# Kernel tuning notes

Measured on AMD Instinct MI355X. Metric: run time of the kernel, lower is better.

The kernel has to match this reference:

```python
import jax, jax.numpy as jnp
import numpy as np

VOCAB = 32000
B, S = 1, 2048
D = 1024          # emb_dim == qkv_dim
H = 16            # num_heads
HD = D // H       # head_dim = 64
M = 4096          # mlp_dim
L = 4             # num_layers
WIN = 512         # sliding_window_size
HALF = WIN // 2   # attend to |i-j| <= HALF
N_GLOBAL = 64
EPS = 1e-6


def sinusoidal_pos_emb(max_len, d, max_scale=10000.0):
    pos = np.arange(max_len)[:, None].astype(np.float32)
    div = np.exp(np.arange(0, d, 2).astype(np.float32) * (-np.log(max_scale) / d))
    pe = np.zeros((max_len, d), dtype=np.float32)
    pe[:, 0::2] = np.sin(pos * div)
    pe[:, 1::2] = np.cos(pos * div)
    return jnp.asarray(pe)


def layer_norm(x, scale, bias):
    mu = jnp.mean(x, axis=-1, keepdims=True)
    var = jnp.mean(jnp.square(x - mu), axis=-1, keepdims=True)
    return (x - mu) * jax.lax.rsqrt(var + EPS) * scale + bias


def setup_inputs() -> dict:
    key = jax.random.key(0)
    ks = jax.random.split(key, 16)
    inputs = jax.random.randint(ks[0], (B, S), 0, VOCAB, dtype=jnp.int32)
    gm = jnp.zeros((B, S), dtype=bool).at[:, :N_GLOBAL].set(True)
    std = 0.02
    return {
        'inputs': inputs,
        'global_mask': gm,
        'embed': jax.random.normal(ks[1], (VOCAB, D), jnp.float32),
        'wq': jax.random.normal(ks[2], (L, D, H, HD), jnp.float32) * std,
        'wk': jax.random.normal(ks[3], (L, D, H, HD), jnp.float32) * std,
        'wv': jax.random.normal(ks[4], (L, D, H, HD), jnp.float32) * std,
        'wo': jax.random.normal(ks[5], (L, H, HD, D), jnp.float32) * std,
        'ln1_s': jnp.ones((L, D), jnp.float32),
        'ln1_b': jnp.zeros((L, D), jnp.float32),
        'ln2_s': jnp.ones((L, D), jnp.float32),
        'ln2_b': jnp.zeros((L, D), jnp.float32),
        'w1': jax.random.normal(ks[6], (L, D, M), jnp.float32) * std,
        'b1': jnp.zeros((L, M), jnp.float32),
        'w2': jax.random.normal(ks[7], (L, M, D), jnp.float32) * std,
        'b2': jnp.zeros((L, D), jnp.float32),
        'lnf_s': jnp.ones((D,), jnp.float32),
        'lnf_b': jnp.zeros((D,), jnp.float32),
    }


def _attention_mask(global_mask):
    idx = jnp.arange(S)
    band = jnp.abs(idx[:, None] - idx[None, :]) <= HALF           # [S, S]
    allowed = band[None, :, :] | global_mask[:, :, None] | global_mask[:, None, :]
    return allowed[:, None, :, :]                                  # [B, 1, S, S]


def forward(inputs, global_mask, embed, wq, wk, wv, wo, ln1_s, ln1_b,
            ln2_s, ln2_b, w1, b1, w2, b2, lnf_s, lnf_b):
    x = embed[inputs]                                # [B, S, D]
    x = x + sinusoidal_pos_emb(S, D)[None]
    mask = _attention_mask(global_mask)              # [B, 1, S, S]
    neg = jnp.asarray(-1e9, x.dtype)
    scale = 1.0 / jnp.sqrt(jnp.asarray(HD, x.dtype))
    for l in range(L):
        h = layer_norm(x, ln1_s[l], ln1_b[l])
        q = jnp.einsum('bsd,dhk->bshk', h, wq[l]) * scale
        k = jnp.einsum('bsd,dhk->bshk', h, wk[l])
        v = jnp.einsum('bsd,dhk->bshk', h, wv[l])
        scores = jnp.einsum('bqhk,bshk->bhqs', q, k)         # [B, H, S, S]
        scores = jnp.where(mask, scores, neg)
        probs = jax.nn.softmax(scores, axis=-1)
        ctx = jnp.einsum('bhqs,bshk->bqhk', probs, v)
        attn_out = jnp.einsum('bqhk,hkd->bqd', ctx, wo[l])
        x = x + attn_out
        y = layer_norm(x, ln2_s[l], ln2_b[l])
        y = jax.nn.relu(jnp.einsum('bsd,dm->bsm', y, w1[l]) + b1[l])
        y = jnp.einsum('bsm,md->bsd', y, w2[l]) + b2[l]
        x = x + y
    return layer_norm(x, lnf_s, lnf_b)


def reference(inputs, global_mask, embed, wq, wk, wv, wo, ln1_s, ln1_b,
              ln2_s, ln2_b, w1, b1, w2, b2, lnf_s, lnf_b):
    return forward(inputs, global_mask, embed, wq, wk, wv, wo, ln1_s, ln1_b,
                   ln2_s, ln2_b, w1, b1, w2, b2, lnf_s, lnf_b)
```

## Files before the change

kernel.cpp:

```cpp
#include <hip/hip_runtime.h>
#include <hip/hip_bf16.h>

typedef __attribute__((ext_vector_type(8))) short bf16x8;
typedef __attribute__((ext_vector_type(4))) float f32x4;

__device__ __forceinline__ ushort f2bf(float f) {
    union { float f; uint u; } v; v.f = f;
    uint r = v.u + 0x7FFF + ((v.u >> 16) & 1);
    return (ushort)(r >> 16);
}

__device__ __forceinline__ void ld16(const void* g, void* l) {
    __builtin_amdgcn_global_load_lds(
        (const __attribute__((address_space(1))) void*)g,
        (__attribute__((address_space(3))) void*)l, 16, 0, 0);
}

__global__ __launch_bounds__(256) void conv_w_kernel(
    const float* __restrict__ src, ushort* __restrict__ dst,
    int K, int N, float scale)
{
    __shared__ ushort Ts[64][65];
    const int tid = threadIdx.x;
    const int n0 = blockIdx.x * 64;
    const int k0 = blockIdx.y * 64;
    const int c4 = tid & 15;
    const int r0 = tid >> 4;
    #pragma unroll
    for (int it = 0; it < 4; it++) {
        int r = r0 + it * 16;
        float4 v = *(const float4*)(src + (size_t)(k0 + r) * N + n0 + c4 * 4);
        Ts[c4 * 4 + 0][r] = f2bf(v.x * scale);
        Ts[c4 * 4 + 1][r] = f2bf(v.y * scale);
        Ts[c4 * 4 + 2][r] = f2bf(v.z * scale);
        Ts[c4 * 4 + 3][r] = f2bf(v.w * scale);
    }
    __syncthreads();
    #pragma unroll
    for (int it = 0; it < 4; it++) {
        int nr = r0 + it * 16;
        uint lo = (uint)Ts[nr][c4 * 4 + 0] | ((uint)Ts[nr][c4 * 4 + 1] << 16);
        uint hi = (uint)Ts[nr][c4 * 4 + 2] | ((uint)Ts[nr][c4 * 4 + 3] << 16);
        uint2 w = make_uint2(lo, hi);
        *(uint2*)(dst + (size_t)(n0 + nr) * K + k0 + c4 * 4) = w;
    }
}

template<int TN>
__global__ __launch_bounds__(256) void gemm_t(
    const ushort* __restrict__ A, const ushort* __restrict__ Bt,
    const float* __restrict__ bias, const float* resid,
    float* outF, ushort* outB, int M, int N, int K, int relu)
{
    __shared__ ushort As[4][128 * 32];
    __shared__ ushort Bs[4][TN * 32];
    const int tid  = threadIdx.x;
    const int lane = tid & 63;
    const int wave = tid >> 6;
    const int quad = lane >> 4;
    const int lr   = lane & 15;
    const int wm   = wave >> 1;
    const int wn   = wave & 1;
    constexpr int NT = (TN == 128) ? 4 : 2;
    const int bm0 = blockIdx.x * 128;
    const int bn0 = blockIdx.y * TN;

    f32x4 acc[4][NT];
    #pragma unroll
    for (int i = 0; i < 4; i++)
        #pragma unroll
        for (int j = 0; j < NT; j++)
            acc[i][j] = (f32x4){0.f, 0.f, 0.f, 0.f};

    const ushort* gA = A  + (size_t)(bm0 + (tid >> 2)) * K + (tid & 3) * 8;
    const ushort* gB = Bt + (size_t)(bn0 + (tid >> 2)) * K + (tid & 3) * 8;

    auto stage = [&](int b, int k) {
        ushort* la = &As[b][wave * 512];
        ushort* lb = &Bs[b][wave * 512];
        ld16(gA + k, la);
        ld16(gA + k + (size_t)64 * K, la + 2048);
        ld16(gB + k, lb);
        if constexpr (TN == 128) ld16(gB + k + (size_t)64 * K, lb + 2048);
    };
    auto step = [&](int b, int t3) {
        bf16x8 aF[4], bF[NT];
        const ushort* as = As[b];
        const ushort* bs = Bs[b];
        #pragma unroll
        for (int mt = 0; mt < 4; mt++)
            aF[mt] = *(const bf16x8*)&as[(wm * 64 + mt * 16 + lr) * 32 + quad * 8];
        #pragma unroll
        for (int nt = 0; nt < NT; nt++)
            bF[nt] = *(const bf16x8*)&bs[(wn * (TN / 2) + nt * 16 + lr) * 32 + quad * 8];
        if (t3 >= 0) stage(t3 & 3, t3 * 32);
        #pragma unroll
        for (int mt = 0; mt < 4; mt++)
            #pragma unroll
            for (int nt = 0; nt < NT; nt++)
                acc[mt][nt] = __builtin_amdgcn_mfma_f32_16x16x32_bf16(
                    aF[mt], bF[nt], acc[mt][nt], 0, 0, 0);
    };

    const int ntk = K >> 5;
    stage(0, 0); stage(1, 32); stage(2, 64);
    for (int t = 0; t < ntk - 2; ++t) {
        if constexpr (TN == 128) asm volatile("s_waitcnt vmcnt(8)" ::: "memory");
        else                     asm volatile("s_waitcnt vmcnt(6)" ::: "memory");
        __builtin_amdgcn_s_barrier();
        step(t & 3, (t + 3 < ntk) ? (t + 3) : -1);
    }
    if constexpr (TN == 128) asm volatile("s_waitcnt vmcnt(4)" ::: "memory");
    else                     asm volatile("s_waitcnt vmcnt(3)" ::: "memory");
    __builtin_amdgcn_s_barrier();
    step((ntk - 2) & 3, -1);
    asm volatile("s_waitcnt vmcnt(0)" ::: "memory");
    __builtin_amdgcn_s_barrier();
    step((ntk - 1) & 3, -1);

    #pragma unroll
    for (int mt = 0; mt < 4; mt++) {
        #pragma unroll
        for (int nt = 0; nt < NT; nt++) {
            int col  = bn0 + wn * (TN / 2) + nt * 16 + lr;
            int rowb = bm0 + wm * 64 + mt * 16 + quad * 4;
            #pragma unroll
            for (int r = 0; r < 4; r++) {
                int row = rowb + r;
                float v = acc[mt][nt][r];
                if (bias)  v += bias[col];
                if (resid) v += resid[(size_t)row * N + col];
                if (relu)  v = fmaxf(v, 0.f);
                if (outF)  outF[(size_t)row * N + col] = v;
                else       outB[(size_t)row * N + col] = f2bf(v);
            }
        }
    }
}

#define LDA 72

__global__ __launch_bounds__(256) void attn_mfma_kernel(
    const ushort* __restrict__ qkv, ushort* __restrict__ Cm,
    float* __restrict__ po, float* __restrict__ pm, float* __restrict__ pl)
{
    const int bx   = blockIdx.x;
    const int h    = blockIdx.y;
    const int sp   = (bx >= 31);
    const int qt   = sp ? 0 : bx + 1;
    const int s    = sp ? bx - 31 : 0;
    const int tid  = threadIdx.x;
    const int lane = tid & 63;
    const int wave = tid >> 6;
    const int quad = lane >> 4;
    const int lr   = lane & 15;
    const int q0   = qt * 64;

    __shared__ ushort Qs[64 * LDA];
    __shared__ ushort Ks[64 * LDA];
    __shared__ ushort Vt[64 * LDA];
    __shared__ ushort Ps[64 * LDA];

    {
        int ql = tid >> 2, d0 = (tid & 3) * 16;
        const ushort* qp = qkv + (size_t)(q0 + ql) * 3072 + h * 64 + d0;
        *(uint4*)&Qs[ql * LDA + d0]     = *(const uint4*)qp;
        *(uint4*)&Qs[ql * LDA + d0 + 8] = *(const uint4*)(qp + 8);
    }
    __syncthreads();

    bf16x8 aQ[2];
    #pragma unroll
    for (int kc = 0; kc < 2; kc++)
        aQ[kc] = *(const bf16x8*)&Qs[(wave * 16 + lr) * LDA + kc * 32 + quad * 8];

    f32x4 o[4];
    #pragma unroll
    for (int nt = 0; nt < 4; nt++) o[nt] = (f32x4){0.f, 0.f, 0.f, 0.f};
    float m_[4], l_[4];
    #pragma unroll
    for (int r = 0; r < 4; r++) { m_[r] = -1e30f; l_[r] = 0.f; }

    int kt0 = 0, kt1 = 0, ntiles;
    if (sp) {
        ntiles = 8;
    } else {
        kt0 = qt - 4; if (kt0 < 1)  kt0 = 1;
        kt1 = qt + 4; if (kt1 > 31) kt1 = 31;
        ntiles = 1 + (kt1 - kt0 + 1);
    }

    for (int idx = 0; idx < ntiles; idx++) {
        int kt, maskF;
        if (sp) { kt = s * 8 + idx; maskF = 0; }
        else if (idx == 0) { kt = 0; maskF = 0; }
        else { kt = kt0 + idx - 1; maskF = (kt == qt - 4) || (kt == qt + 4); }

        __syncthreads();

        {
            int kl = tid >> 2, d0 = (tid & 3) * 16;
            const ushort* kp = qkv + (size_t)(kt * 64 + kl) * 3072 + 1024 + h * 64 + d0;
            *(uint4*)&Ks[kl * LDA + d0]     = *(const uint4*)kp;
            *(uint4*)&Ks[kl * LDA + d0 + 8] = *(const uint4*)(kp + 8);
        }
        {
            int kp2 = tid & 31, dc = tid >> 5, d0v = dc * 8;
            const ushort* vp = qkv + (size_t)(kt * 64 + 2 * kp2) * 3072 + 2048 + h * 64 + d0v;
            ushort va[8], vb[8];
            *(uint4*)va = *(const uint4*)vp;
            *(uint4*)vb = *(const uint4*)(vp + 3072);
            #pragma unroll
            for (int i = 0; i < 8; i++) {
                uint w = (uint)va[i] | ((uint)vb[i] << 16);
                *(uint*)&Vt[(d0v + i) * LDA + 2 * kp2] = w;
            }
        }
        __syncthreads();

        f32x4 sAcc[4];
        #pragma unroll
        for (int nt = 0; nt < 4; nt++) sAcc[nt] = (f32x4){0.f, 0.f, 0.f, 0.f};
        #pragma unroll
        for (int kc = 0; kc < 2; kc++) {
            #pragma unroll
            for (int nt = 0; nt < 4; nt++) {
                bf16x8 bK = *(const bf16x8*)&Ks[(nt * 16 + lr) * LDA + kc * 32 + quad * 8];
                sAcc[nt] = __builtin_amdgcn_mfma_f32_16x16x32_bf16(aQ[kc], bK, sAcc[nt], 0, 0, 0);
            }
        }

        if (maskF) {
            #pragma unroll
            for (int nt = 0; nt < 4; nt++) {
                int j = kt * 64 + lr + nt * 16;
                #pragma unroll
                for (int r = 0; r < 4; r++) {
                    int q = q0 + wave * 16 + quad * 4 + r;
                    int d = q - j; if (d < 0) d = -d;
                    if (d > 256) sAcc[nt][r] = -1e30f;
                }
            }
        }

        float rmax[4];
        #pragma unroll
        for (int r = 0; r < 4; r++) {
            float v = fmaxf(fmaxf(sAcc[0][r], sAcc[1][r]), fmaxf(sAcc[2][r], sAcc[3][r]));
            v = fmaxf(v, __shfl_xor(v, 1));
            v = fmaxf(v, __shfl_xor(v, 2));
            v = fmaxf(v, __shfl_xor(v, 4));
            v = fmaxf(v, __shfl_xor(v, 8));
            rmax[r] = v;
        }
        float alpha[4];
        #pragma unroll
        for (int r = 0; r < 4; r++) {
            float mn = fmaxf(m_[r], rmax[r]);
            alpha[r] = __expf(m_[r] - mn);
            m_[r] = mn;
        }
        float psum[4] = {0.f, 0.f, 0.f, 0.f};
        #pragma unroll
        for (int nt = 0; nt < 4; nt++)
            #pragma unroll
            for (int r = 0; r < 4; r++) {
                float p = __expf(sAcc[nt][r] - m_[r]);
                sAcc[nt][r] = p;
                psum[r] += p;
            }
        #pragma unroll
        for (int r = 0; r < 4; r++) {
            float v = psum[r];
            v += __shfl_xor(v, 1);
            v += __shfl_xor(v, 2);
            v += __shfl_xor(v, 4);
            v += __shfl_xor(v, 8);
            l_[r] = l_[r] * alpha[r] + v;
        }
        #pragma unroll
        for (int nt = 0; nt < 4; nt++)
            #pragma unroll
            for (int r = 0; r < 4; r++)
                o[nt][r] *= alpha[r];

        #pragma unroll
        for (int nt = 0; nt < 4; nt++)
            #pragma unroll
            for (int r = 0; r < 4; r++)
                Ps[(wave * 16 + quad * 4 + r) * LDA + lr + nt * 16] = f2bf(sAcc[nt][r]);
        __syncthreads();

        #pragma unroll
        for (int kc = 0; kc < 2; kc++) {
            bf16x8 aP = *(const bf16x8*)&Ps[(wave * 16 + lr) * LDA + kc * 32 + quad * 8];
            #pragma unroll
            for (int nt = 0; nt < 4; nt++) {
                bf16x8 bV = *(const bf16x8*)&Vt[(nt * 16 + lr) * LDA + kc * 32 + quad * 8];
                o[nt] = __builtin_amdgcn_mfma_f32_16x16x32_bf16(aP, bV, o[nt], 0, 0, 0);
            }
        }
    }

    if (!sp) {
        #pragma unroll
        for (int nt = 0; nt < 4; nt++) {
            int dim = lr + nt * 16;
            #pragma unroll
            for (int r = 0; r < 4; r++) {
                int row = q0 + wave * 16 + quad * 4 + r;
                Cm[(size_t)row * 1024 + h * 64 + dim] = f2bf(o[nt][r] / l_[r]);
            }
        }
    } else {
        const int base = (h * 4 + s) * 64;
        #pragma unroll
        for (int nt = 0; nt < 4; nt++) {
            int dim = lr + nt * 16;
            #pragma unroll
            for (int r = 0; r < 4; r++) {
                int row = wave * 16 + quad * 4 + r;
                po[(size_t)(base + row) * 64 + dim] = o[nt][r];
            }
        }
        if (lr == 0) {
            #pragma unroll
            for (int r = 0; r < 4; r++) {
                int row = wave * 16 + quad * 4 + r;
                pm[base + row] = m_[r];
                pl[base + row] = l_[r];
            }
        }
    }
}

__global__ __launch_bounds__(256) void attn_combine_kernel(
    const float* __restrict__ po, const float* __restrict__ pm,
    const float* __restrict__ pl, ushort* __restrict__ Cm)
{
    const int h   = blockIdx.x;
    const int tid = threadIdx.x;
    const int row = tid >> 2;
    const int d0  = (tid & 3) * 16;
    float m[4], l[4];
    #pragma unroll
    for (int s = 0; s < 4; s++) {
        m[s] = pm[(h * 4 + s) * 64 + row];
        l[s] = pl[(h * 4 + s) * 64 + row];
    }
    float M = fmaxf(fmaxf(m[0], m[1]), fmaxf(m[2], m[3]));
    float w[4], L = 0.f;
    #pragma unroll
    for (int s = 0; s < 4; s++) { w[s] = __expf(m[s] - M); L += l[s] * w[s]; }
    float inv = 1.0f / L;
    #pragma unroll
    for (int dd = 0; dd < 16; dd += 4) {
        float a0 = 0.f, a1 = 0.f, a2 = 0.f, a3 = 0.f;
        #pragma unroll
        for (int s = 0; s < 4; s++) {
            float4 v = *(const float4*)&po[(size_t)((h * 4 + s) * 64 + row) * 64 + d0 + dd];
            a0 += v.x * w[s]; a1 += v.y * w[s]; a2 += v.z * w[s]; a3 += v.w * w[s];
        }
        ushort* out = &Cm[(size_t)row * 1024 + h * 64 + d0 + dd];
        out[0] = f2bf(a0 * inv); out[1] = f2bf(a1 * inv);
        out[2] = f2bf(a2 * inv); out[3] = f2bf(a3 * inv);
    }
}

__global__ __launch_bounds__(256) void ln_kernel(
    const float* __restrict__ X, const float* __restrict__ gs,
    const float* __restrict__ gb, ushort* outB, float* outF)
{
    const int row = blockIdx.x;
    const int tid = threadIdx.x;
    const int lane = tid & 63;
    const int wave = tid >> 6;
    __shared__ float red[8];

    const float* x = X + (size_t)row * 1024;
    float4 v = *(const float4*)(x + tid * 4);
    float s1 = v.x + v.y + v.z + v.w;
    float s2 = v.x * v.x + v.y * v.y + v.z * v.z + v.w * v.w;
    #pragma unroll
    for (int off = 32; off > 0; off >>= 1) {
        s1 += __shfl_down(s1, off);
        s2 += __shfl_down(s2, off);
    }
    if (lane == 0) { red[wave] = s1; red[4 + wave] = s2; }
    __syncthreads();
    float S1 = red[0] + red[1] + red[2] + red[3];
    float S2 = red[4] + red[5] + red[6] + red[7];
    float mu  = S1 * (1.0f / 1024.0f);
    float var = S2 * (1.0f / 1024.0f) - mu * mu;
    float inv = rsqrtf(var + 1e-6f);
    const float* vp = (const float*)&v;
    #pragma unroll
    for (int i = 0; i < 4; i++) {
        int d = tid * 4 + i;
        float val = (vp[i] - mu) * inv * gs[d] + gb[d];
        if (outF) outF[(size_t)row * 1024 + d] = val;
        else      outB[(size_t)row * 1024 + d] = f2bf(val);
    }
}

__global__ __launch_bounds__(256) void embed_kernel(
    const int* __restrict__ ids, const float* __restrict__ emb,
    float* __restrict__ x)
{
    const int row = blockIdx.x;
    const int tid = threadIdx.x;
    const int id  = ids[row];
    const float c = 0.0089944731f;
    #pragma unroll
    for (int i = 0; i < 4; i++) {
        int d  = tid * 4 + i;
        int de = d & ~1;
        float dv  = __expf(-c * (float)de);
        float ang = (float)row * dv;
        float pe  = (d & 1) ? cosf(ang) : sinf(ang);
        x[(size_t)row * 1024 + d] = emb[(size_t)id * 1024 + d] + pe;
    }
}

extern "C" void kernel_launch(void* const* d_in, const int* in_sizes, int n_in,
                              void* d_out, int out_size, void* d_ws, size_t ws_size,
                              hipStream_t stream)
{
    const int*   ids   = (const int*)d_in[0];
    const float* embed = (const float*)d_in[2];
    const float* wq    = (const float*)d_in[3];
    const float* wk    = (const float*)d_in[4];
    const float* wv    = (const float*)d_in[5];
    const float* wo    = (const float*)d_in[6];
    const float* ln1s  = (const float*)d_in[7];
    const float* ln1b  = (const float*)d_in[8];
    const float* ln2s  = (const float*)d_in[9];
    const float* ln2b  = (const float*)d_in[10];
    const float* w1    = (const float*)d_in[11];
    const float* b1    = (const float*)d_in[12];
    const float* w2    = (const float*)d_in[13];
    const float* b2    = (const float*)d_in[14];
    const float* lnfs  = (const float*)d_in[15];
    const float* lnfb  = (const float*)d_in[16];

    char* ws = (char*)d_ws;
    float*  x   = (float*)ws;
    ushort* h   = (ushort*)(ws + (size_t)(8  << 20));
    ushort* qkv = (ushort*)(ws + (size_t)(12 << 20));
    ushort* ctx = (ushort*)(ws + (size_t)(24 << 20));
    ushort* wb  = (ushort*)(ws + (size_t)(28 << 20));
    float*  po  = (float*)(ws + (size_t)(8  << 20));
    float*  pm  = (float*)(ws + (size_t)(9  << 20));
    float*  pl  = (float*)(ws + (size_t)(9  << 20) + (1 << 16));
    ushort* y1  = qkv;

    const dim3 blk(256);

    embed_kernel<<<2048, blk, 0, stream>>>(ids, embed, x);

    for (int l = 0; l < 4; l++) {
        const float* wq_l = wq + (size_t)l * 1024 * 1024;
        const float* wk_l = wk + (size_t)l * 1024 * 1024;
        const float* wv_l = wv + (size_t)l * 1024 * 1024;
        const float* wo_l = wo + (size_t)l * 1024 * 1024;
        const float* w1_l = w1 + (size_t)l * 1024 * 4096;
        const float* w2_l = w2 + (size_t)l * 4096 * 1024;

        ln_kernel<<<2048, blk, 0, stream>>>(x, ln1s + l * 1024, ln1b + l * 1024, h, nullptr);

        conv_w_kernel<<<dim3(16, 16), blk, 0, stream>>>(wq_l, wb,                1024, 1024, 0.125f);
        conv_w_kernel<<<dim3(16, 16), blk, 0, stream>>>(wk_l, wb + 1024 * 1024,  1024, 1024, 1.0f);
        conv_w_kernel<<<dim3(16, 16), blk, 0, stream>>>(wv_l, wb + 2048 * 1024,  1024, 1024, 1.0f);
        gemm_t<128><<<dim3(16, 24), blk, 0, stream>>>(h, wb, nullptr, nullptr,
                                                      nullptr, qkv, 2048, 3072, 1024, 0);

        attn_mfma_kernel<<<dim3(35, 16), blk, 0, stream>>>(qkv, ctx, po, pm, pl);
        attn_combine_kernel<<<dim3(16), blk, 0, stream>>>(po, pm, pl, ctx);

        conv_w_kernel<<<dim3(16, 16), blk, 0, stream>>>(wo_l, wb, 1024, 1024, 1.0f);
        gemm_t<64><<<dim3(16, 16), blk, 0, stream>>>(ctx, wb, nullptr, x,
                                                     x, nullptr, 2048, 1024, 1024, 0);

        ln_kernel<<<2048, blk, 0, stream>>>(x, ln2s + l * 1024, ln2b + l * 1024, h, nullptr);

        conv_w_kernel<<<dim3(64, 16), blk, 0, stream>>>(w1_l, wb, 1024, 4096, 1.0f);
        gemm_t<128><<<dim3(16, 32), blk, 0, stream>>>(h, wb, b1 + (size_t)l * 4096, nullptr,
                                                      nullptr, y1, 2048, 4096, 1024, 1);

        conv_w_kernel<<<dim3(16, 64), blk, 0, stream>>>(w2_l, wb, 4096, 1024, 1.0f);
        gemm_t<64><<<dim3(16, 16), blk, 0, stream>>>(y1, wb, b2 + (size_t)l * 1024, x,
                                                     x, nullptr, 2048, 1024, 4096, 0);
    }

    ln_kernel<<<2048, blk, 0, stream>>>(x, lnfs, lnfb, nullptr, (float*)d_out);
}
```

Before: 1.151 ms.

## Split-K the output-projection and MLP-down GEMMs with a separate reduction kernel

The N=1024 GEMMs (attention output projection and second MLP matmul) launched only 256 blocks. They now split K across blockIdx.z (2 and 4 ways) and write fp32 partials to a workspace buffer. A new reduction kernel sums the partials and adds bias and the residual. This raises block count to fill more CUs, at the cost of extra partial-sum traffic and one more launch per GEMM.

```diff
diff --git a/kernel.cpp b/kernel.cpp
--- a/kernel.cpp
+++ b/kernel.cpp
@@ -50,7 +50,8 @@
 __global__ __launch_bounds__(256) void gemm_t(
     const ushort* __restrict__ A, const ushort* __restrict__ Bt,
     const float* __restrict__ bias, const float* resid,
-    float* outF, ushort* outB, int M, int N, int K, int relu)
+    float* outF, ushort* outB, int M, int N, int K, int ldk, int relu,
+    float* __restrict__ outP)
 {
     __shared__ ushort As[4][128 * 32];
     __shared__ ushort Bs[4][TN * 32];
@@ -64,6 +65,7 @@
     constexpr int NT = (TN == 128) ? 4 : 2;
     const int bm0 = blockIdx.x * 128;
     const int bn0 = blockIdx.y * TN;
+    const int kz  = blockIdx.z * K;
 
     f32x4 acc[4][NT];
     #pragma unroll
@@ -72,16 +74,16 @@
         for (int j = 0; j < NT; j++)
             acc[i][j] = (f32x4){0.f, 0.f, 0.f, 0.f};
 
-    const ushort* gA = A  + (size_t)(bm0 + (tid >> 2)) * K + (tid & 3) * 8;
-    const ushort* gB = Bt + (size_t)(bn0 + (tid >> 2)) * K + (tid & 3) * 8;
+    const ushort* gA = A  + (size_t)(bm0 + (tid >> 2)) * ldk + kz + (tid & 3) * 8;
+    const ushort* gB = Bt + (size_t)(bn0 + (tid >> 2)) * ldk + kz + (tid & 3) * 8;
 
     auto stage = [&](int b, int k) {
         ushort* la = &As[b][wave * 512];
         ushort* lb = &Bs[b][wave * 512];
         ld16(gA + k, la);
-        ld16(gA + k + (size_t)64 * K, la + 2048);
+        ld16(gA + k + (size_t)64 * ldk, la + 2048);
         ld16(gB + k, lb);
-        if constexpr (TN == 128) ld16(gB + k + (size_t)64 * K, lb + 2048);
+        if constexpr (TN == 128) ld16(gB + k + (size_t)64 * ldk, lb + 2048);
     };
     auto step = [&](int b, int t3) {
         bf16x8 aF[4], bF[NT];
@@ -117,6 +119,22 @@
     asm volatile("s_waitcnt vmcnt(0)" ::: "memory");
     __builtin_amdgcn_s_barrier();
     step((ntk - 1) & 3, -1);
+
+    if (outP) {
+        float* dst = outP + (size_t)blockIdx.z * M * N;
+        #pragma unroll
+        for (int mt = 0; mt < 4; mt++) {
+            #pragma unroll
+            for (int nt = 0; nt < NT; nt++) {
+                int col  = bn0 + wn * (TN / 2) + nt * 16 + lr;
+                int rowb = bm0 + wm * 64 + mt * 16 + quad * 4;
+                #pragma unroll
+                for (int r = 0; r < 4; r++)
+                    dst[(size_t)(rowb + r) * N + col] = acc[mt][nt][r];
+            }
+        }
+        return;
+    }
 
     #pragma unroll
     for (int mt = 0; mt < 4; mt++) {
@@ -136,6 +154,31 @@
             }
         }
     }
+}
+
+__global__ __launch_bounds__(256) void reduceK_kernel(
+    const float* __restrict__ part, int nsplit,
+    const float* __restrict__ bias, const float* __restrict__ resid,
+    float* __restrict__ outF, int N)
+{
+    const int row = blockIdx.x;
+    const int col = threadIdx.x * 4;
+    const size_t off = (size_t)row * N + col;
+    const size_t stride = (size_t)2048 * N;
+    float4 a = *(const float4*)(part + off);
+    for (int s = 1; s < nsplit; s++) {
+        float4 b = *(const float4*)(part + (size_t)s * stride + off);
+        a.x += b.x; a.y += b.y; a.z += b.z; a.w += b.w;
+    }
+    if (bias) {
+        a.x += bias[col]; a.y += bias[col + 1];
+        a.z += bias[col + 2]; a.w += bias[col + 3];
+    }
+    if (resid) {
+        float4 r = *(const float4*)(resid + off);
+        a.x += r.x; a.y += r.y; a.z += r.z; a.w += r.w;
+    }
+    *(float4*)(outF + off) = a;
 }
 
 #define LDA 72
@@ -452,6 +495,7 @@
     float*  po  = (float*)(ws + (size_t)(8  << 20));
     float*  pm  = (float*)(ws + (size_t)(9  << 20));
     float*  pl  = (float*)(ws + (size_t)(9  << 20) + (1 << 16));
+    float*  pK  = (float*)(ws + (size_t)(40 << 20));
     ushort* y1  = qkv;
 
     const dim3 blk(256);
@@ -472,24 +516,26 @@
         conv_w_kernel<<<dim3(16, 16), blk, 0, stream>>>(wk_l, wb + 1024 * 1024,  1024, 1024, 1.0f);
         conv_w_kernel<<<dim3(16, 16), blk, 0, stream>>>(wv_l, wb + 2048 * 1024,  1024, 1024, 1.0f);
         gemm_t<128><<<dim3(16, 24), blk, 0, stream>>>(h, wb, nullptr, nullptr,
-                                                      nullptr, qkv, 2048, 3072, 1024, 0);
+                                                      nullptr, qkv, 2048, 3072, 1024, 1024, 0, nullptr);
 
         attn_mfma_kernel<<<dim3(35, 16), blk, 0, stream>>>(qkv, ctx, po, pm, pl);
         attn_combine_kernel<<<dim3(16), blk, 0, stream>>>(po, pm, pl, ctx);
 
         conv_w_kernel<<<dim3(16, 16), blk, 0, stream>>>(wo_l, wb, 1024, 1024, 1.0f);
-        gemm_t<64><<<dim3(16, 16), blk, 0, stream>>>(ctx, wb, nullptr, x,
-                                                     x, nullptr, 2048, 1024, 1024, 0);
+        gemm_t<64><<<dim3(16, 16, 2), blk, 0, stream>>>(ctx, wb, nullptr, nullptr,
+                                                        nullptr, nullptr, 2048, 1024, 512, 1024, 0, pK);
+        reduceK_kernel<<<2048, blk, 0, stream>>>(pK, 2, nullptr, x, x, 1024);
 
         ln_kernel<<<2048, blk, 0, stream>>>(x, ln2s + l * 1024, ln2b + l * 1024, h, nullptr);
 
         conv_w_kernel<<<dim3(64, 16), blk, 0, stream>>>(w1_l, wb, 1024, 4096, 1.0f);
         gemm_t<128><<<dim3(16, 32), blk, 0, stream>>>(h, wb, b1 + (size_t)l * 4096, nullptr,
-                                                      nullptr, y1, 2048, 4096, 1024, 1);
+                                                      nullptr, y1, 2048, 4096, 1024, 1024, 1, nullptr);
 
         conv_w_kernel<<<dim3(16, 64), blk, 0, stream>>>(w2_l, wb, 4096, 1024, 1.0f);
-        gemm_t<64><<<dim3(16, 16), blk, 0, stream>>>(y1, wb, b2 + (size_t)l * 1024, x,
-                                                     x, nullptr, 2048, 1024, 4096, 0);
+        gemm_t<64><<<dim3(16, 16, 4), blk, 0, stream>>>(y1, wb, nullptr, nullptr,
+                                                        nullptr, nullptr, 2048, 1024, 1024, 4096, 0, pK);
+        reduceK_kernel<<<2048, blk, 0, stream>>>(pK, 4, b2 + (size_t)l * 1024, x, x, 1024);
     }
 
     ln_kernel<<<2048, blk, 0, stream>>>(x, lnfs, lnfb, nullptr, (float*)d_out);
```

Result: faster. 1.071 ms (-7.0%).
